# Kernel optimization log

Hardware: AMD Instinct MI355X
Metric: run time of the kernel (lower is better)

## Reference

```python
import jax, jax.numpy as jnp
import numpy as np

T, B, D, H, O = 128, 256, 512, 1024, 1


def setup_inputs() -> dict:
    key = jax.random.key(0)
    ks = jax.random.split(key, 10)
    s_in = 1.0 / np.sqrt(D)
    s_h = 1.0 / np.sqrt(H)
    u = lambda k, shape, s: jax.random.uniform(k, shape, jnp.float32, -s, s)
    return {
        "inputs": jax.random.normal(ks[0], (T, B, D), jnp.float32),
        "hidden_state": jnp.zeros((1, B, H), jnp.float32),
        "cell_state": jnp.zeros((1, B, H), jnp.float32),
        "W1": u(ks[1], (H, D), s_in),
        "b1": u(ks[2], (H,), s_in),
        "W_ih": u(ks[3], (4 * H, H), s_h),
        "W_hh": u(ks[4], (4 * H, H), s_h),
        "b_ih": u(ks[5], (4 * H,), s_h),
        "b_hh": u(ks[6], (4 * H,), s_h),
        "W_out": u(ks[7], (O, H), s_h),
        "b_out": u(ks[8], (O,), s_h),
    }


def reference(inputs, hidden_state, cell_state, W1, b1, W_ih, W_hh, b_ih, b_hh, W_out, b_out):
    # first_layer + ReLU (dropout is identity in eval mode)
    x = jax.nn.relu(jnp.einsum("tbd,hd->tbh", inputs, W1) + b1)  # (T,B,H)
    # Precompute input contribution to all gates for every timestep.
    xg = jnp.einsum("tbh,gh->tbg", x, W_ih) + b_ih + b_hh  # (T,B,4H)
    h0 = hidden_state[0]
    c0 = cell_state[0]

    def step(carry, xg_t):
        h, c = carry
        g = xg_t + h @ W_hh.T  # (B,4H), PyTorch gate order i,f,g,o
        i, f, gg, o = jnp.split(g, 4, axis=-1)
        i = jax.nn.sigmoid(i)
        f = jax.nn.sigmoid(f)
        gg = jnp.tanh(gg)
        o = jax.nn.sigmoid(o)
        c = f * c + i * gg
        h = o * jnp.tanh(c)
        return (h, c), h

    (hT, cT), hs = jax.lax.scan(step, (h0, c0), xg)
    out = jnp.einsum("tbh,oh->tbo", hs, W_out) + b_out  # (T,B,O)
    return out, hT[None], cT[None]
```

## Files before the change

kernel.cpp:

```cpp
#include <hip/hip_runtime.h>
#include <hip/hip_bf16.h>
#include <math.h>


#define T_STEPS 128
#define BATCH   256
#define DIM     512
#define HID     1024
#define GATES   4096
#define FPAD    32

typedef __attribute__((ext_vector_type(8))) short short8;
typedef __attribute__((ext_vector_type(4))) float f4;
typedef __attribute__((ext_vector_type(4))) int i4;

__device__ __forceinline__ short f2bf(float f) {
    union { float f; unsigned u; } x; x.f = f;
    unsigned r = (x.u + 0x7fffu + ((x.u >> 16) & 1u)) >> 16;
    return (short)r;
}
__device__ __forceinline__ float bf2f(short s) {
    union { unsigned u; float f; } x; x.u = ((unsigned)(unsigned short)s) << 16;
    return x.f;
}
__device__ __forceinline__ float sigm(float x) { return 1.f / (1.f + __expf(-x)); }
__device__ __forceinline__ float tanh_fast(float x) { return 2.f / (1.f + __expf(-2.f * x)) - 1.f; }

__device__ __forceinline__ void gll16(const void* g, void* l) {
    __builtin_amdgcn_global_load_lds(
        (const __attribute__((address_space(1))) void*)g,
        (__attribute__((address_space(3))) void*)l, 16, 0, 0);
}
__device__ __forceinline__ void store16_wt(void* p, i4 v) {
    asm volatile("global_store_dwordx4 %0, %1, off sc0 sc1"
                 :: "v"(p), "v"(v) : "memory");
}

__global__ __launch_bounds__(256) void cvt_f32_bf16(const float* __restrict__ in,
                                                    short* __restrict__ out, int n4) {
    int i = blockIdx.x * 256 + threadIdx.x;
    if (i < n4) {
        float4 v = ((const float4*)in)[i];
        union { short s[4]; long long ll; } r;
        r.s[0] = f2bf(v.x); r.s[1] = f2bf(v.y); r.s[2] = f2bf(v.z); r.s[3] = f2bf(v.w);
        ((long long*)out)[i] = r.ll;
    }
}

__global__ __launch_bounds__(256) void cvt_h0_blocked(const float* __restrict__ h0,
                                                      short* __restrict__ dst) {
    int b = blockIdx.x, k0 = threadIdx.x * 4;
    float4 v = *(const float4*)&h0[(size_t)b * HID + k0];
    union { short s[4]; long long ll; } p;
    p.s[0] = f2bf(v.x); p.s[1] = f2bf(v.y); p.s[2] = f2bf(v.z); p.s[3] = f2bf(v.w);
    *(long long*)&dst[(k0 >> 3) * (BATCH * 8) + b * 8 + (k0 & 7)] = p.ll;
}

__global__ __launch_bounds__(256) void cvt_permute_rows(const float* __restrict__ in,
                                                        short* __restrict__ out) {
    int r = blockIdx.x;
    int hc = r >> 2, g = r & 3;
    const float* src = in + (size_t)(g * HID + hc) * HID;
    short* dst = out + (size_t)r * HID;
    int c = threadIdx.x * 4;
    float4 v = *(const float4*)&src[c];
    union { short s[4]; long long ll; } p;
    p.s[0] = f2bf(v.x); p.s[1] = f2bf(v.y); p.s[2] = f2bf(v.z); p.s[3] = f2bf(v.w);
    *(long long*)&dst[c] = p.ll;
}

__global__ __launch_bounds__(256) void bias_sum_perm(const float* __restrict__ a,
                                                     const float* __restrict__ b,
                                                     float* __restrict__ o) {
    int r = blockIdx.x * 256 + threadIdx.x;
    int hc = r >> 2, g = r & 3;
    int src = g * HID + hc;
    o[r] = a[src] + b[src];
}

__global__ __launch_bounds__(256) void copy_f32v4(const float* __restrict__ in,
                                                  float* __restrict__ out, int n4) {
    int i = blockIdx.x * 256 + threadIdx.x;
    if (i < n4) ((float4*)out)[i] = ((const float4*)in)[i];
}

__global__ __launch_bounds__(256) void zero_i32(int* __restrict__ p, int n) {
    for (int i = blockIdx.x * 256 + threadIdx.x; i < n; i += gridDim.x * 256)
        p[i] = 0;
}

__global__ __launch_bounds__(256) void gemm_bt(const short* __restrict__ A,
                                               const short* __restrict__ B,
                                               const float* __restrict__ bias,
                                               short* __restrict__ C,
                                               int M, int N, int K, int do_relu) {
    __shared__ __align__(16) short As[128 * 32];
    __shared__ __align__(16) short Bs[128 * 32];
    const int tid = threadIdx.x, wave = tid >> 6, lane = tid & 63;
    const int wm = (wave >> 1) * 64, wn = (wave & 1) * 64;

    const int flat = blockIdx.y * gridDim.x + blockIdx.x;
    const int cpx = (gridDim.x * gridDim.y) >> 3;
    const int swz = (flat & 7) * cpx + (flat >> 3);
    const int bm = (swz % gridDim.x) * 128, bn = (swz / gridDim.x) * 128;

    const int sr = lane >> 2, sc = (lane & 3) * 8;

    f4 acc[4][4] = {};

    for (int k0 = 0; k0 < K; k0 += 32) {
        __syncthreads();
#pragma unroll
        for (int j = 0; j < 2; ++j) {
            int c = wave * 2 + j;
            gll16(&A[(size_t)(bm + c * 16 + sr) * K + k0 + sc], &As[c * 512]);
            gll16(&B[(size_t)(bn + c * 16 + sr) * K + k0 + sc], &Bs[c * 512]);
        }
        __syncthreads();
        short8 af[4], bfr[4];
#pragma unroll
        for (int i = 0; i < 4; ++i) {
            af[i]  = *(const short8*)&As[(wm + i * 16 + (lane & 15)) * 32 + (lane >> 4) * 8];
            bfr[i] = *(const short8*)&Bs[(wn + i * 16 + (lane & 15)) * 32 + (lane >> 4) * 8];
        }
#pragma unroll
        for (int i = 0; i < 4; ++i)
#pragma unroll
            for (int j = 0; j < 4; ++j)
                acc[i][j] = __builtin_amdgcn_mfma_f32_16x16x32_bf16(af[i], bfr[j], acc[i][j], 0, 0, 0);
    }

    const int lc = lane & 15, lr = (lane >> 4) * 4;
#pragma unroll
    for (int i = 0; i < 4; ++i) {
#pragma unroll
        for (int j = 0; j < 4; ++j) {
            int col = bn + wn + j * 16 + lc;
            float bv = bias[col];
#pragma unroll
            for (int r = 0; r < 4; ++r) {
                int row = bm + wm + i * 16 + lr + r;
                float v = acc[i][j][r] + bv;
                if (do_relu) v = fmaxf(v, 0.f);
                C[(size_t)row * N + col] = f2bf(v);
            }
        }
    }
}

__global__ __launch_bounds__(256) void lstm_persist(const short* __restrict__ Whh,
                                                    const short* __restrict__ xgc,
                                                    short* __restrict__ hist,
                                                    float* __restrict__ cf,
                                                    float* __restrict__ hT,
                                                    float* __restrict__ cT,
                                                    int* __restrict__ flags,
                                                    int* __restrict__ go,
                                                    int TC, int last) {
    __shared__ __align__(16) short Bf[32768];
    __shared__ __align__(16) short Ht[512];
    const int tid = threadIdx.x, w = tid >> 6, lane = tid & 63;
    const int bg = blockIdx.x >> 7, cg = blockIdx.x & 127;
    const int bb = bg * 64, hc0 = cg * 8;
    const int hcl = lane & 7, gp = (lane >> 3) & 1, q = lane >> 4;

#pragma unroll
    for (int i = 0; i < 16; ++i) {
        int p = w * 16 + i;
        int c = p >> 1, t = p & 1;
        gll16(&Whh[(size_t)((t * 2 + gp) * HID + hc0 + hcl) * HID + c * 32 + q * 8],
              &Bf[p * 512]);
    }

    const int rowb = bb + w * 16 + q * 4 + gp * 2;
    float creg[2];
#pragma unroll
    for (int e = 0; e < 2; ++e)
        creg[e] = cf[(size_t)(rowb + e) * HID + hc0 + hcl];

    __syncthreads();

    unsigned long long xw[2], xwn[2];
#pragma unroll
    for (int e = 0; e < 2; ++e)
        xw[e] = *(const unsigned long long*)&xgc[(size_t)(rowb + e) * GATES
                                                 + (hc0 + hcl) * 4];

#define ISSUE_A(buf, g)                                                        \
    _Pragma("unroll")                                                          \
    for (int i = 0; i < 8; ++i)                                                \
        buf[i] = *(const short8*)(abase + (size_t)((g) * 8 + i) * astr);

#define COMPUTE_A(buf, g)                                                      \
    __builtin_amdgcn_s_setprio(1);                                             \
    _Pragma("unroll")                                                          \
    for (int i = 0; i < 8; ++i) {                                              \
        short8 b0 = *(const short8*)&Bf[(((g) * 8 + i) * 2 + 0) * 512 + lane * 8]; \
        short8 b1 = *(const short8*)&Bf[(((g) * 8 + i) * 2 + 1) * 512 + lane * 8]; \
        acc0 = __builtin_amdgcn_mfma_f32_16x16x32_bf16(buf[i], b0, acc0, 0, 0, 0); \
        acc1 = __builtin_amdgcn_mfma_f32_16x16x32_bf16(buf[i], b1, acc1, 0, 0, 0); \
    }                                                                          \
    __builtin_amdgcn_s_setprio(0);

    for (int tt = 0; tt < TC; ++tt) {
        if (tt + 1 < TC) {
#pragma unroll
            for (int e = 0; e < 2; ++e)
                xwn[e] = *(const unsigned long long*)&xgc[(size_t)((tt + 1) * BATCH + rowb + e) * GATES
                                                          + (hc0 + hcl) * 4];
        }

        const short* abase = hist + (size_t)tt * BATCH * HID
                           + (size_t)q * (BATCH * 8) + (size_t)(bb + w * 16 + (lane & 15)) * 8;
        const size_t astr = (size_t)4 * (BATCH * 8);
        f4 acc0 = {}, acc1 = {};
        short8 ab0[8], ab1[8], ab2[8];
        ISSUE_A(ab0, 0)
        ISSUE_A(ab1, 1)
        ISSUE_A(ab2, 2)
        COMPUTE_A(ab0, 0)
        ISSUE_A(ab0, 3)
        COMPUTE_A(ab1, 1)
        COMPUTE_A(ab2, 2)
        COMPUTE_A(ab0, 3)

        float p0[4], p1[4];
#pragma unroll
        for (int r = 0; r < 4; ++r) {
            p0[r] = __shfl_xor(acc0[r], 8);
            p1[r] = __shfl_xor(acc1[r], 8);
        }

        int glast = last && (tt == TC - 1);
#pragma unroll
        for (int e = 0; e < 2; ++e) {
            int r = gp * 2 + e;
            size_t b = rowb + e;
            float gi = gp ? p0[r] : acc0[r];
            float gf = gp ? acc0[r] : p0[r];
            float gg = gp ? p1[r] : acc1[r];
            float go_ = gp ? acc1[r] : p1[r];
            gi += bf2f((short)(xw[e] & 0xffff));
            gf += bf2f((short)((xw[e] >> 16) & 0xffff));
            gg += bf2f((short)((xw[e] >> 32) & 0xffff));
            go_ += bf2f((short)((xw[e] >> 48) & 0xffff));
            float si = sigm(gi), sf = sigm(gf), tg = tanh_fast(gg), so = sigm(go_);
            float cn = sf * creg[e] + si * tg;
            float hv = so * tanh_fast(cn);
            creg[e] = cn;
            Ht[(w * 16 + q * 4 + gp * 2 + e) * 8 + hcl] = f2bf(hv);
            if (glast) {
                hT[b * HID + hc0 + hcl] = hv;
                cT[b * HID + hc0 + hcl] = cn;
            }
        }
        xw[0] = xwn[0]; xw[1] = xwn[1];
        __syncthreads();

        short* hn = hist + (size_t)(tt + 1) * BATCH * HID
                  + (size_t)cg * (BATCH * 8) + (size_t)bb * 8;
        if (tid < 64)
            store16_wt(&hn[tid * 8], *(const i4*)&Ht[tid * 8]);

        if (tt < TC - 1) {
            __syncthreads();
            const int base = (tt * 4 + bg) * 128 * FPAD;
            if (tid == 0)
                __hip_atomic_store(&flags[base + cg * FPAD], 1,
                                   __ATOMIC_RELAXED, __HIP_MEMORY_SCOPE_AGENT);
            if (cg == 0) {
                if (tid < 128) {
                    while (__hip_atomic_load(&flags[base + tid * FPAD],
                                             __ATOMIC_RELAXED, __HIP_MEMORY_SCOPE_AGENT) == 0)
                        __builtin_amdgcn_s_sleep(1);
                }
                __syncthreads();
                if (tid == 0)
                    __hip_atomic_store(&go[(tt * 4 + bg) * FPAD], 1,
                                       __ATOMIC_RELAXED, __HIP_MEMORY_SCOPE_AGENT);
            } else {
                if (tid == 0) {
                    while (__hip_atomic_load(&go[(tt * 4 + bg) * FPAD],
                                             __ATOMIC_RELAXED, __HIP_MEMORY_SCOPE_AGENT) == 0)
                        __builtin_amdgcn_s_sleep(1);
                }
                __syncthreads();
            }
        }
    }

#undef ISSUE_A
#undef COMPUTE_A

#pragma unroll
    for (int e = 0; e < 2; ++e)
        cf[(size_t)(rowb + e) * HID + hc0 + hcl] = creg[e];
}

__global__ __launch_bounds__(256) void out_head(const short* __restrict__ hs,
                                                const float* __restrict__ Wout,
                                                const float* __restrict__ bout,
                                                float* __restrict__ out) {
    int row = blockIdx.x * 4 + (threadIdx.x >> 6);
    int lane = threadIdx.x & 63;
    int tt = row >> 8, b = row & 255;
    const short* sb = hs + (size_t)(tt + 1) * BATCH * HID + b * 8;
    const float2* w2 = (const float2*)Wout;
    float s = 0.f;
#pragma unroll
    for (int j = 0; j < 8; ++j) {
        int m = j * 64 + lane;
        int pk = *(const int*)&sb[(size_t)(m >> 2) * (BATCH * 8) + 2 * (m & 3)];
        float2 wv = w2[m];
        union { unsigned u; float f; } lo, hi;
        lo.u = ((unsigned)pk) << 16;
        hi.u = ((unsigned)pk) & 0xffff0000u;
        s += lo.f * wv.x + hi.f * wv.y;
    }
#pragma unroll
    for (int off = 32; off; off >>= 1) s += __shfl_down(s, off);
    if (lane == 0) out[row] = s + bout[0];
}

extern "C" void kernel_launch(void* const* d_in, const int* in_sizes, int n_in,
                              void* d_out, int out_size, void* d_ws, size_t ws_size,
                              hipStream_t stream) {
    const float* inputs = (const float*)d_in[0];
    const float* h0     = (const float*)d_in[1];
    const float* c0     = (const float*)d_in[2];
    const float* W1     = (const float*)d_in[3];
    const float* b1     = (const float*)d_in[4];
    const float* W_ih   = (const float*)d_in[5];
    const float* W_hh   = (const float*)d_in[6];
    const float* b_ih   = (const float*)d_in[7];
    const float* b_hh   = (const float*)d_in[8];
    const float* W_out  = (const float*)d_in[9];
    const float* b_out  = (const float*)d_in[10];

    float* out = (float*)d_out;
    float* hT  = out + (size_t)T_STEPS * BATCH;
    float* cT  = hT + (size_t)BATCH * HID;

    char* base = (char*)d_ws;
    size_t off = 0;
    auto alloc = [&](size_t bytes) -> char* {
        char* q = base + off;
        off += (bytes + 255) & ~(size_t)255;
        return q;
    };
    short* W1b   = (short*)alloc((size_t)HID * DIM * 2);
    short* Wihb  = (short*)alloc((size_t)GATES * HID * 2);
    short* Whhb  = (short*)alloc((size_t)GATES * HID * 2);
    float* biasf = (float*)alloc((size_t)GATES * 4);
    float* cf    = (float*)alloc((size_t)BATCH * HID * 4);
    int*   flags = (int*)alloc((size_t)T_STEPS * 4 * 128 * FPAD * 4);
    int*   go    = (int*)alloc((size_t)T_STEPS * 4 * FPAD * 4);

    short* inb_a = (short*)alloc((size_t)T_STEPS * BATCH * DIM * 2);
    short* xb_a  = (short*)alloc((size_t)T_STEPS * BATCH * HID * 2);

    size_t per_t = (size_t)BATCH * GATES * 2 + (size_t)BATCH * HID * 2;
    int TC = 32;
    while (TC > 1 && off + (size_t)TC * per_t + (size_t)BATCH * HID * 2 + 65536 > ws_size)
        TC >>= 1;

    short* hhist = (short*)alloc((size_t)(TC + 1) * BATCH * HID * 2);
    short* xgb_c = (short*)alloc((size_t)TC * BATCH * GATES * 2);

    cvt_f32_bf16<<<(HID * DIM / 4 + 255) / 256, 256, 0, stream>>>(W1, W1b, HID * DIM / 4);
    cvt_permute_rows<<<GATES, 256, 0, stream>>>(W_ih, Wihb);
    cvt_f32_bf16<<<(GATES * HID / 4 + 255) / 256, 256, 0, stream>>>(W_hh, Whhb, GATES * HID / 4);
    bias_sum_perm<<<GATES / 256, 256, 0, stream>>>(b_ih, b_hh, biasf);
    cvt_h0_blocked<<<BATCH, 256, 0, stream>>>(h0, hhist);
    copy_f32v4<<<(BATCH * HID / 4 + 255) / 256, 256, 0, stream>>>(c0, cf, BATCH * HID / 4);
    zero_i32<<<512, 256, 0, stream>>>(flags, T_STEPS * 4 * 128 * FPAD + T_STEPS * 4 * FPAD);

    {
        int Ma = T_STEPS * BATCH;
        cvt_f32_bf16<<<(Ma * DIM / 4 + 255) / 256, 256, 0, stream>>>(
            inputs, inb_a, Ma * DIM / 4);
        gemm_bt<<<dim3(Ma / 128, HID / 128), 256, 0, stream>>>(
            inb_a, W1b, b1, xb_a, Ma, HID, DIM, 1);
    }

    for (int t0 = 0; t0 < T_STEPS; t0 += TC) {
        int Mc = TC * BATCH;
        int last = (t0 + TC >= T_STEPS);
        gemm_bt<<<dim3(Mc / 128, GATES / 128), 256, 0, stream>>>(
            xb_a + (size_t)t0 * BATCH * HID, Wihb, biasf, xgb_c,
            Mc, GATES, HID, 0);

        lstm_persist<<<512, 256, 0, stream>>>(Whhb, xgb_c, hhist, cf, hT, cT,
                                              flags + (size_t)t0 * 4 * 128 * FPAD,
                                              go + (size_t)t0 * 4 * FPAD,
                                              TC, last);

        out_head<<<TC * BATCH / 4, 256, 0, stream>>>(hhist, W_out, b_out,
                                                     out + (size_t)t0 * BATCH);
        copy_f32v4<<<(BATCH * HID * 2 / 16 + 255) / 256, 256, 0, stream>>>(
            (const float*)(hhist + (size_t)TC * BATCH * HID), (float*)hhist,
            BATCH * HID * 2 / 16);
    }
}
```

Baseline: 1.337 ms.

## Double-buffer GEMM LDS tiles with BK=64, XOR swizzle and priority hints

Replaces the single-buffered BK=32 bf16 GEMM with a double-buffered BK=64 version that prefetches the next K tile while MFMAs consume the current one, removing one barrier per iteration. LDS rows are XOR-swizzled to avoid bank conflicts on the fragment reads, and s_setprio is raised around the MFMA block. The XCD remap now also handles tile counts not divisible by 8. This raises LDS use to 64KB per block, which may lower occupancy, in exchange for overlapping loads with compute in the input-projection GEMMs.

```diff
diff --git a/kernel.cpp b/kernel.cpp
--- a/kernel.cpp
+++ b/kernel.cpp
@@ -89,46 +89,70 @@
         p[i] = 0;
 }
 
-__global__ __launch_bounds__(256) void gemm_bt(const short* __restrict__ A,
-                                               const short* __restrict__ B,
-                                               const float* __restrict__ bias,
-                                               short* __restrict__ C,
-                                               int M, int N, int K, int do_relu) {
-    __shared__ __align__(16) short As[128 * 32];
-    __shared__ __align__(16) short Bs[128 * 32];
+__global__ __launch_bounds__(256) void gemm_bt2(const short* __restrict__ A,
+                                                const short* __restrict__ B,
+                                                const float* __restrict__ bias,
+                                                short* __restrict__ C,
+                                                int M, int N, int K, int do_relu) {
+    __shared__ __align__(16) short As[2][128 * 64];
+    __shared__ __align__(16) short Bs[2][128 * 64];
     const int tid = threadIdx.x, wave = tid >> 6, lane = tid & 63;
     const int wm = (wave >> 1) * 64, wn = (wave & 1) * 64;
 
+    const int nwg = gridDim.x * gridDim.y;
     const int flat = blockIdx.y * gridDim.x + blockIdx.x;
-    const int cpx = (gridDim.x * gridDim.y) >> 3;
-    const int swz = (flat & 7) * cpx + (flat >> 3);
+    const int qq = nwg >> 3, rr = nwg & 7;
+    const int xcd = flat & 7, oin = flat >> 3;
+    const int swz = (xcd < rr ? xcd * (qq + 1) : rr * (qq + 1) + (xcd - rr) * qq) + oin;
     const int bm = (swz % gridDim.x) * 128, bn = (swz / gridDim.x) * 128;
 
-    const int sr = lane >> 2, sc = (lane & 3) * 8;
+#define STAGE2(bufi, kt)                                                       \
+    {                                                                          \
+        const int k0_ = (kt) * 64;                                             \
+        _Pragma("unroll")                                                      \
+        for (int u = 0; u < 4; ++u) {                                          \
+            int r0 = wave * 32 + u * 8;                                        \
+            int row = r0 + (lane >> 3);                                        \
+            int kof = ((lane & 7) ^ (row & 7)) * 8;                            \
+            gll16(&A[(size_t)(bm + row) * K + k0_ + kof], &As[bufi][r0 * 64]); \
+            gll16(&B[(size_t)(bn + row) * K + k0_ + kof], &Bs[bufi][r0 * 64]); \
+        }                                                                      \
+    }
 
     f4 acc[4][4] = {};
-
-    for (int k0 = 0; k0 < K; k0 += 32) {
+    const int NT = K >> 6;
+
+    STAGE2(0, 0)
+    __syncthreads();
+
+    int cur = 0;
+    for (int kt = 0; kt < NT; ++kt) {
+        if (kt + 1 < NT) STAGE2(cur ^ 1, kt + 1)
+
+#pragma unroll
+        for (int ks = 0; ks < 2; ++ks) {
+            short8 af[4], bfr[4];
+#pragma unroll
+            for (int i = 0; i < 4; ++i) {
+                int ra = wm + i * 16 + (lane & 15);
+                int sa = (ks * 4 + (lane >> 4)) ^ (ra & 7);
+                af[i] = *(const short8*)&As[cur][ra * 64 + sa * 8];
+                int rb = wn + i * 16 + (lane & 15);
+                int sb = (ks * 4 + (lane >> 4)) ^ (rb & 7);
+                bfr[i] = *(const short8*)&Bs[cur][rb * 64 + sb * 8];
+            }
+            __builtin_amdgcn_s_setprio(1);
+#pragma unroll
+            for (int i = 0; i < 4; ++i)
+#pragma unroll
+                for (int j = 0; j < 4; ++j)
+                    acc[i][j] = __builtin_amdgcn_mfma_f32_16x16x32_bf16(af[i], bfr[j], acc[i][j], 0, 0, 0);
+            __builtin_amdgcn_s_setprio(0);
+        }
         __syncthreads();
-#pragma unroll
-        for (int j = 0; j < 2; ++j) {
-            int c = wave * 2 + j;
-            gll16(&A[(size_t)(bm + c * 16 + sr) * K + k0 + sc], &As[c * 512]);
-            gll16(&B[(size_t)(bn + c * 16 + sr) * K + k0 + sc], &Bs[c * 512]);
-        }
-        __syncthreads();
-        short8 af[4], bfr[4];
-#pragma unroll
-        for (int i = 0; i < 4; ++i) {
-            af[i]  = *(const short8*)&As[(wm + i * 16 + (lane & 15)) * 32 + (lane >> 4) * 8];
-            bfr[i] = *(const short8*)&Bs[(wn + i * 16 + (lane & 15)) * 32 + (lane >> 4) * 8];
-        }
-#pragma unroll
-        for (int i = 0; i < 4; ++i)
-#pragma unroll
-            for (int j = 0; j < 4; ++j)
-                acc[i][j] = __builtin_amdgcn_mfma_f32_16x16x32_bf16(af[i], bfr[j], acc[i][j], 0, 0, 0);
-    }
+        cur ^= 1;
+    }
+#undef STAGE2
 
     const int lc = lane & 15, lr = (lane >> 4) * 4;
 #pragma unroll
@@ -379,14 +403,14 @@
         int Ma = T_STEPS * BATCH;
         cvt_f32_bf16<<<(Ma * DIM / 4 + 255) / 256, 256, 0, stream>>>(
             inputs, inb_a, Ma * DIM / 4);
-        gemm_bt<<<dim3(Ma / 128, HID / 128), 256, 0, stream>>>(
+        gemm_bt2<<<dim3(Ma / 128, HID / 128), 256, 0, stream>>>(
             inb_a, W1b, b1, xb_a, Ma, HID, DIM, 1);
     }
 
     for (int t0 = 0; t0 < T_STEPS; t0 += TC) {
         int Mc = TC * BATCH;
         int last = (t0 + TC >= T_STEPS);
-        gemm_bt<<<dim3(Mc / 128, GATES / 128), 256, 0, stream>>>(
+        gemm_bt2<<<dim3(Mc / 128, GATES / 128), 256, 0, stream>>>(
             xb_a + (size_t)t0 * BATCH * HID, Wihb, biasf, xgb_c,
             Mc, GATES, HID, 0);
 
```

Result: no change. 1.321 ms (-1.2%).
